# Kernel tuning notes

Hardware: AMD Instinct MI355X
Metric: run time of the kernel (lower is better)

The kernel has to match this reference:

```python
import jax, jax.numpy as jnp
import numpy as np

B, T, N, O = 128, 256, 64, 32
E, H = 32, 64            # embed_dim, hyper_dim
S = O * 4 + 1            # state_dim = 129


def setup_inputs() -> dict:
    key = jax.random.key(0)
    ks = jax.random.split(key, 16)
    def lin(k, i, o):
        return jax.random.normal(k, (i, o), jnp.float32) * (1.0 / np.sqrt(i))
    inp = {}
    inp["agent_qs"] = jax.random.normal(ks[0], (B, T, N), jnp.float32)
    inp["obs"] = jax.random.normal(ks[1], (B, T, N, O), jnp.float32)
    inp["agent_mask"] = jax.random.randint(ks[2], (B, N), 0, 2).astype(jnp.int32)
    # hyper_w_1: Linear(S,H) -> ReLU -> Linear(H, N*E)
    inp["w1_1"] = lin(ks[3], S, H); inp["b1_1"] = jnp.zeros((H,), jnp.float32)
    inp["w1_2"] = lin(ks[4], H, N * E); inp["b1_2"] = jnp.zeros((N * E,), jnp.float32)
    # hyper_w_2: Linear(S,H) -> ReLU -> Linear(H, E)
    inp["w2_1"] = lin(ks[5], S, H); inp["b2_1"] = jnp.zeros((H,), jnp.float32)
    inp["w2_2"] = lin(ks[6], H, E); inp["b2_2"] = jnp.zeros((E,), jnp.float32)
    # hyper_b_1: Linear(S,E)
    inp["wb1"] = lin(ks[7], S, E); inp["bb1"] = jnp.zeros((E,), jnp.float32)
    # hyper_b_2: Linear(S,E) -> ReLU -> Linear(E,1)
    inp["wb2_1"] = lin(ks[8], S, E); inp["bb2_1"] = jnp.zeros((E,), jnp.float32)
    inp["wb2_2"] = lin(ks[9], E, 1); inp["bb2_2"] = jnp.zeros((1,), jnp.float32)
    return inp


def _state_features(obs, agent_mask):
    # Faithful to torch loop: stats over the FIRST k agents where k = mask.sum().
    b, t, n, o = obs.shape
    k = agent_mask.sum(axis=1)                                   # [B]
    am = (jnp.arange(n)[None, :] < k[:, None]).astype(obs.dtype)  # [B,N]
    m = am[:, None, :, None]                                      # [B,1,N,1]
    cnt = k.astype(obs.dtype)[:, None, None]                      # [B,1,1]
    safe = jnp.maximum(cnt, 1.0)
    mean = (obs * m).sum(axis=2) / safe                           # [B,T,O]
    var = (((obs - mean[:, :, None, :]) ** 2) * m).sum(axis=2) / jnp.maximum(cnt - 1.0, 1.0)
    std = jnp.where(cnt > 1.0, jnp.sqrt(var), 0.0)                # unbiased std, 0 if k<=1
    mb = m > 0
    mn = jnp.where(mb, obs, jnp.inf).min(axis=2)
    mx = jnp.where(mb, obs, -jnp.inf).max(axis=2)
    ratio = jnp.broadcast_to(cnt / n, (b, t, 1))
    feats = jnp.concatenate([mean, std, mn, mx, ratio], axis=-1)  # [B,T,S]
    return jnp.where(cnt > 0.0, feats, 0.0)                       # rows stay zero if k==0


def reference(agent_qs, obs, agent_mask,
              w1_1, b1_1, w1_2, b1_2,
              w2_1, b2_1, w2_2, b2_2,
              wb1, bb1, wb2_1, bb2_1, wb2_2, bb2_2):
    b, t, n = agent_qs.shape
    e = wb1.shape[1]
    states = _state_features(obs, agent_mask)                     # [B,T,S]
    s = states.reshape(b * t, -1)                                 # [BT,S]
    qs = agent_qs.reshape(b * t, n)                               # [BT,N]
    w1 = jnp.abs(jax.nn.relu(s @ w1_1 + b1_1) @ w1_2 + b1_2).reshape(b * t, n, e)
    b1 = s @ wb1 + bb1                                            # [BT,E]
    hidden = jax.nn.elu(jnp.einsum('bn,bne->be', qs, w1) + b1)    # [BT,E]
    w2 = jnp.abs(jax.nn.relu(s @ w2_1 + b2_1) @ w2_2 + b2_2)      # [BT,E]
    b2 = jax.nn.relu(s @ wb2_1 + bb2_1) @ wb2_2 + bb2_2           # [BT,1]
    q_tot = (hidden * w2).sum(axis=-1, keepdims=True) + b2        # [BT,1]
    return q_tot.reshape(b, t, 1)
```

## Files before the change

kernel.cpp:

```cpp
#include <hip/hip_runtime.h>
#include <math.h>

#define BB 128
#define TT 256
#define NN 64
#define OO 32
#define EE 32
#define HH 64
#define SS 129
#define BT 32768
#define SP 132

__global__ __launch_bounds__(256) void k_states(const float* __restrict__ obs,
                                                const int* __restrict__ mask,
                                                float* __restrict__ states) {
    int w = threadIdx.x >> 6;
    int l = threadIdx.x & 63;
    int bt = blockIdx.x * 4 + w;
    int b = bt >> 8;

    int kv = mask[(b << 6) + l];
    #pragma unroll
    for (int off = 32; off; off >>= 1) kv += __shfl_xor(kv, off);

    int o = l & 31, nh = l >> 5;
    float sum = 0.f, ssq = 0.f, mn = INFINITY, mx = -INFINITY;
    const float* op = obs + ((size_t)bt << 11);
    for (int n = nh; n < kv; n += 2) {
        float v = op[(n << 5) + o];
        sum += v;
        ssq = fmaf(v, v, ssq);
        mn = fminf(mn, v);
        mx = fmaxf(mx, v);
    }
    sum += __shfl_xor(sum, 32);
    ssq += __shfl_xor(ssq, 32);
    mn = fminf(mn, __shfl_xor(mn, 32));
    mx = fmaxf(mx, __shfl_xor(mx, 32));

    float kf = (float)kv;
    float mean = sum / fmaxf(kf, 1.f);
    float var = (ssq - kf * mean * mean) / fmaxf(kf - 1.f, 1.f);
    float sd = (kv > 1) ? sqrtf(fmaxf(var, 0.f)) : 0.f;
    if (kv == 0) { mean = 0.f; sd = 0.f; mn = 0.f; mx = 0.f; }

    float* sp = states + (size_t)bt * SP;
    if (l < 32) {
        sp[o] = mean;
        sp[32 + o] = sd;
        sp[64 + o] = mn;
        sp[96 + o] = mx;
    }
    if (l == 0) {
        sp[128] = kf * 0.015625f;
        sp[129] = 0.f; sp[130] = 0.f; sp[131] = 0.f;
    }
}

__global__ __launch_bounds__(256) void k_mlp1(const float* __restrict__ states,
        const float* __restrict__ w1_1, const float* __restrict__ b1_1,
        const float* __restrict__ w2_1, const float* __restrict__ b2_1,
        const float* __restrict__ wb1,  const float* __restrict__ bb1,
        const float* __restrict__ wb2_1,const float* __restrict__ bb2_1,
        float* __restrict__ h1, float* __restrict__ t2,
        float* __restrict__ b1v, float* __restrict__ t3) {
    __shared__ float wl[SP * 192];
    __shared__ float bl[192];
    int t = threadIdx.x;

    for (int idx = t; idx < SP * 192; idx += 256) {
        int k = idx / 192;
        int c = idx - k * 192;
        float v = 0.f;
        if (k < SS) {
            if (c < 64)       v = w1_1[k * 64 + c];
            else if (c < 128) v = w2_1[k * 64 + c - 64];
            else if (c < 160) v = wb1[k * 32 + c - 128];
            else              v = wb2_1[k * 32 + c - 160];
        }
        wl[idx] = v;
    }
    if (t < 192) {
        float v;
        if (t < 64)       v = b1_1[t];
        else if (t < 128) v = b2_1[t - 64];
        else if (t < 160) v = bb1[t - 128];
        else              v = bb2_1[t - 160];
        bl[t] = v;
    }
    __syncthreads();

    int cg = t & 7, rg = t >> 3;
    int c0 = cg * 24;
    int row0 = blockIdx.x * 128 + rg * 4;
    float acc[4][24];
    #pragma unroll
    for (int i = 0; i < 4; i++)
        #pragma unroll
        for (int j = 0; j < 24; j++) acc[i][j] = 0.f;

    const float* s0 = states + (size_t)row0 * SP;
    for (int k0 = 0; k0 < SP; k0 += 4) {
        float4 sv[4];
        #pragma unroll
        for (int i = 0; i < 4; i++) sv[i] = *(const float4*)(s0 + i * SP + k0);
        #pragma unroll
        for (int kk = 0; kk < 4; kk++) {
            float wv[24];
            #pragma unroll
            for (int q = 0; q < 6; q++)
                *(float4*)&wv[q * 4] = *(const float4*)&wl[(k0 + kk) * 192 + c0 + q * 4];
            #pragma unroll
            for (int i = 0; i < 4; i++) {
                float s = ((const float*)&sv[i])[kk];
                #pragma unroll
                for (int j = 0; j < 24; j++) acc[i][j] = fmaf(s, wv[j], acc[i][j]);
            }
        }
    }

    #pragma unroll
    for (int i = 0; i < 4; i++) {
        int row = row0 + i;
        #pragma unroll
        for (int j = 0; j < 24; j++) {
            int c = c0 + j;
            float v = acc[i][j] + bl[c];
            if (c < 128 || c >= 160) v = fmaxf(v, 0.f);
            if (c < 64)       h1[(size_t)row * 64 + c] = v;
            else if (c < 128) t2[(size_t)row * 64 + c - 64] = v;
            else if (c < 160) b1v[(size_t)row * 32 + c - 128] = v;
            else              t3[(size_t)row * 32 + c - 160] = v;
        }
    }
}

__global__ __launch_bounds__(256) void k_w2(const float* __restrict__ t2,
        const float* __restrict__ t3, const float* __restrict__ w2_2,
        const float* __restrict__ b2_2, const float* __restrict__ wb2_2,
        const float* __restrict__ bb2_2,
        float* __restrict__ w2, float* __restrict__ b2v) {
    __shared__ float wl[64 * 32];
    __shared__ float wb[32];
    __shared__ float bb[32];
    int t = threadIdx.x;
    for (int idx = t; idx < 2048; idx += 256) wl[idx] = w2_2[idx];
    if (t < 32) wb[t] = wb2_2[t];
    if (t >= 32 && t < 64) bb[t - 32] = b2_2[t - 32];
    __syncthreads();

    int r = t >> 2, eq = t & 3;
    int row = blockIdx.x * 64 + r;
    int e0 = eq * 8;
    float acc[8];
    #pragma unroll
    for (int j = 0; j < 8; j++) acc[j] = 0.f;

    const float* tp = t2 + (size_t)row * 64;
    for (int h4 = 0; h4 < 64; h4 += 4) {
        float4 tv = *(const float4*)(tp + h4);
        #pragma unroll
        for (int hh = 0; hh < 4; hh++) {
            float s = ((const float*)&tv)[hh];
            float4 wv0 = *(const float4*)&wl[(h4 + hh) * 32 + e0];
            float4 wv1 = *(const float4*)&wl[(h4 + hh) * 32 + e0 + 4];
            acc[0] = fmaf(s, wv0.x, acc[0]); acc[1] = fmaf(s, wv0.y, acc[1]);
            acc[2] = fmaf(s, wv0.z, acc[2]); acc[3] = fmaf(s, wv0.w, acc[3]);
            acc[4] = fmaf(s, wv1.x, acc[4]); acc[5] = fmaf(s, wv1.y, acc[5]);
            acc[6] = fmaf(s, wv1.z, acc[6]); acc[7] = fmaf(s, wv1.w, acc[7]);
        }
    }
    #pragma unroll
    for (int j = 0; j < 8; j++)
        w2[(size_t)row * 32 + e0 + j] = fabsf(acc[j] + bb[e0 + j]);

    if (eq == 0) {
        const float* t3p = t3 + (size_t)row * 32;
        float a = 0.f;
        #pragma unroll
        for (int q = 0; q < 8; q++) {
            float4 v3 = *(const float4*)(t3p + q * 4);
            float4 wv = *(const float4*)&wb[q * 4];
            a = fmaf(v3.x, wv.x, a); a = fmaf(v3.y, wv.y, a);
            a = fmaf(v3.z, wv.z, a); a = fmaf(v3.w, wv.w, a);
        }
        b2v[row] = a + bb2_2[0];
    }
}

__global__ __launch_bounds__(256, 1) void k_main(
        const float* __restrict__ h1g, const float* __restrict__ qsg,
        const float* __restrict__ w12, const float* __restrict__ b12,
        const float* __restrict__ b1vg, const float* __restrict__ w2g,
        const float* __restrict__ b2vg, float* __restrict__ out) {
    __shared__ float sm[36864];
    float* h1T = sm;
    float* Wp  = sm + 8192;
    float* qsT = sm + 24576;
    float* hid = sm + 32768;

    int t = threadIdx.x;
    int row0 = blockIdx.x * 128;

    {
        int r = t >> 1, h0 = (t & 1) * 32;
        const float* hp = h1g + (size_t)(row0 + r) * 64 + h0;
        const float* qp = qsg + (size_t)(row0 + r) * 64 + h0;
        #pragma unroll
        for (int q = 0; q < 8; q++) {
            float4 hv = *(const float4*)(hp + q * 4);
            float4 qv = *(const float4*)(qp + q * 4);
            int hb = h0 + q * 4;
            h1T[(hb + 0) * 128 + r] = hv.x; h1T[(hb + 1) * 128 + r] = hv.y;
            h1T[(hb + 2) * 128 + r] = hv.z; h1T[(hb + 3) * 128 + r] = hv.w;
            qsT[(hb + 0) * 128 + r] = qv.x; qsT[(hb + 1) * 128 + r] = qv.y;
            qsT[(hb + 2) * 128 + r] = qv.z; qsT[(hb + 3) * 128 + r] = qv.w;
        }
    }

    int rg = t >> 4, cg = t & 15;
    int n_l = cg >> 1, eh = cg & 1;
    int r0 = rg * 8;
    int e0 = eh * 16;
    int jbase = n_l * 32 + e0;
    int xorc = n_l << 2;

    float hacc[8][16];
    #pragma unroll
    for (int i = 0; i < 8; i++)
        #pragma unroll
        for (int jj = 0; jj < 16; jj++) hacc[i][jj] = 0.f;

    for (int p = 0; p < 8; ++p) {
        __syncthreads();
        {
            int c4 = (t & 63) * 4;
            int hh0 = t >> 6;
            int csw = c4 ^ (((c4 >> 5) & 7) << 2);
            const float* wsrc = w12 + (size_t)hh0 * 2048 + p * 256 + c4;
            #pragma unroll
            for (int hh = 0; hh < 16; ++hh) {
                float4 wv = *(const float4*)(wsrc + (size_t)hh * 4 * 2048);
                *(float4*)&Wp[(hh * 4 + hh0) * 256 + csw] = wv;
            }
        }
        __syncthreads();

        int n = p * 8 + n_l;
        float c[8][16];
        {
            float biasv[16];
            #pragma unroll
            for (int q = 0; q < 4; q++)
                *(float4*)&biasv[q * 4] = *(const float4*)(b12 + n * 32 + e0 + q * 4);
            #pragma unroll
            for (int i = 0; i < 8; i++)
                #pragma unroll
                for (int jj = 0; jj < 16; jj++) c[i][jj] = biasv[jj];
        }

        #pragma unroll 2
        for (int k = 0; k < 64; k++) {
            float a[8], w[16];
            *(float4*)&a[0] = *(const float4*)&h1T[k * 128 + r0];
            *(float4*)&a[4] = *(const float4*)&h1T[k * 128 + r0 + 4];
            #pragma unroll
            for (int q = 0; q < 4; q++) {
                int j = (jbase + q * 4) ^ xorc;
                *(float4*)&w[q * 4] = *(const float4*)&Wp[k * 256 + j];
            }
            #pragma unroll
            for (int i = 0; i < 8; i++)
                #pragma unroll
                for (int jj = 0; jj < 16; jj++)
                    c[i][jj] = fmaf(a[i], w[jj], c[i][jj]);
        }

        float qv[8];
        *(float4*)&qv[0] = *(const float4*)&qsT[n * 128 + r0];
        *(float4*)&qv[4] = *(const float4*)&qsT[n * 128 + r0 + 4];
        #pragma unroll
        for (int i = 0; i < 8; i++)
            #pragma unroll
            for (int jj = 0; jj < 16; jj++)
                hacc[i][jj] = fmaf(qv[i], fabsf(c[i][jj]), hacc[i][jj]);
    }

    #pragma unroll
    for (int i = 0; i < 8; i++)
        #pragma unroll
        for (int jj = 0; jj < 16; jj++) {
            float v = hacc[i][jj];
            v += __shfl_xor(v, 2);
            v += __shfl_xor(v, 4);
            v += __shfl_xor(v, 8);
            hacc[i][jj] = v;
        }

    if (n_l == 0) {
        #pragma unroll
        for (int i = 0; i < 8; i++)
            #pragma unroll
            for (int q = 0; q < 4; q++) {
                float4 v = make_float4(hacc[i][q * 4], hacc[i][q * 4 + 1],
                                       hacc[i][q * 4 + 2], hacc[i][q * 4 + 3]);
                *(float4*)&hid[(r0 + i) * 32 + e0 + q * 4] = v;
            }
    }
    __syncthreads();

    {
        int r = t >> 1, half = t & 1, he0 = half * 16;
        int row = row0 + r;
        const float* b1p = b1vg + (size_t)row * 32 + he0;
        const float* w2p = w2g + (size_t)row * 32 + he0;
        float accp = 0.f;
        #pragma unroll
        for (int q = 0; q < 4; q++) {
            float4 hv = *(const float4*)&hid[r * 32 + he0 + q * 4];
            float4 bv = *(const float4*)(b1p + q * 4);
            float4 wv = *(const float4*)(w2p + q * 4);
            float x;
            x = hv.x + bv.x; x = x > 0.f ? x : expm1f(x); accp = fmaf(x, wv.x, accp);
            x = hv.y + bv.y; x = x > 0.f ? x : expm1f(x); accp = fmaf(x, wv.y, accp);
            x = hv.z + bv.z; x = x > 0.f ? x : expm1f(x); accp = fmaf(x, wv.z, accp);
            x = hv.w + bv.w; x = x > 0.f ? x : expm1f(x); accp = fmaf(x, wv.w, accp);
        }
        accp += __shfl_xor(accp, 1);
        if (half == 0) out[row] = accp + b2vg[row];
    }
}

extern "C" void kernel_launch(void* const* d_in, const int* in_sizes, int n_in,
                              void* d_out, int out_size, void* d_ws, size_t ws_size,
                              hipStream_t stream) {
    const float* agent_qs = (const float*)d_in[0];
    const float* obs      = (const float*)d_in[1];
    const int*   agent_mask = (const int*)d_in[2];
    const float* w1_1 = (const float*)d_in[3];
    const float* b1_1 = (const float*)d_in[4];
    const float* w1_2 = (const float*)d_in[5];
    const float* b1_2 = (const float*)d_in[6];
    const float* w2_1 = (const float*)d_in[7];
    const float* b2_1 = (const float*)d_in[8];
    const float* w2_2 = (const float*)d_in[9];
    const float* b2_2 = (const float*)d_in[10];
    const float* wb1  = (const float*)d_in[11];
    const float* bb1  = (const float*)d_in[12];
    const float* wb2_1 = (const float*)d_in[13];
    const float* bb2_1 = (const float*)d_in[14];
    const float* wb2_2 = (const float*)d_in[15];
    const float* bb2_2 = (const float*)d_in[16];

    float* ws = (float*)d_ws;
    float* states = ws;
    float* h1  = states + (size_t)BT * SP;
    float* t2  = h1  + (size_t)BT * 64;
    float* b1v = t2  + (size_t)BT * 64;
    float* t3  = b1v + (size_t)BT * 32;
    float* w2  = t3  + (size_t)BT * 32;
    float* b2v = w2  + (size_t)BT * 32;
    float* outp = (float*)d_out;

    k_states<<<BT / 4, 256, 0, stream>>>(obs, agent_mask, states);
    k_mlp1<<<BT / 128, 256, 0, stream>>>(states, w1_1, b1_1, w2_1, b2_1,
                                         wb1, bb1, wb2_1, bb2_1, h1, t2, b1v, t3);
    k_w2<<<BT / 64, 256, 0, stream>>>(t2, t3, w2_2, b2_2, wb2_2, bb2_2, w2, b2v);
    k_main<<<BT / 128, 256, 0, stream>>>(h1, agent_qs, w1_2, b1_2, b1v, w2, b2v, outp);
}
```

Baseline: 611.5 us.

## Shrink per-block tiles in mlp1 and main kernels to raise occupancy

Splits k_mlp1 across a second grid dimension so each block computes 96 output columns instead of 192, which halves LDS and register use and allows 3 blocks per CU. Restructures k_main to process 64 rows per block with 4x4 register tiles and 2 agents per pass (32 passes), dropping the qs transpose and LDS swizzle and reading qs directly from global memory. The aim is higher occupancy for better latency hiding. In exchange the weight tiles are reloaded more often, states are read twice, and each thread reuses fewer operands.

```diff
diff --git a/kernel.cpp b/kernel.cpp
--- a/kernel.cpp
+++ b/kernel.cpp
@@ -57,64 +57,62 @@
     }
 }
 
-__global__ __launch_bounds__(256) void k_mlp1(const float* __restrict__ states,
+__global__ __launch_bounds__(256, 3) void k_mlp1(const float* __restrict__ states,
         const float* __restrict__ w1_1, const float* __restrict__ b1_1,
         const float* __restrict__ w2_1, const float* __restrict__ b2_1,
         const float* __restrict__ wb1,  const float* __restrict__ bb1,
         const float* __restrict__ wb2_1,const float* __restrict__ bb2_1,
         float* __restrict__ h1, float* __restrict__ t2,
         float* __restrict__ b1v, float* __restrict__ t3) {
-    __shared__ float wl[SP * 192];
-    __shared__ float bl[192];
+    __shared__ float wl[SP * 96];
+    __shared__ float bl[96];
     int t = threadIdx.x;
-
-    for (int idx = t; idx < SP * 192; idx += 256) {
-        int k = idx / 192;
-        int c = idx - k * 192;
+    int half = blockIdx.y;
+
+    const float* wA = half ? w2_1 : w1_1;
+    const float* wB = half ? wb2_1 : wb1;
+    const float* bA = half ? b2_1 : b1_1;
+    const float* bB = half ? bb2_1 : bb1;
+    float* outA = half ? t2 : h1;
+    float* outB = half ? t3 : b1v;
+    int reluB = half;
+
+    for (int idx = t; idx < SP * 96; idx += 256) {
+        int k = idx / 96;
+        int c = idx - k * 96;
         float v = 0.f;
-        if (k < SS) {
-            if (c < 64)       v = w1_1[k * 64 + c];
-            else if (c < 128) v = w2_1[k * 64 + c - 64];
-            else if (c < 160) v = wb1[k * 32 + c - 128];
-            else              v = wb2_1[k * 32 + c - 160];
-        }
+        if (k < SS) v = (c < 64) ? wA[k * 64 + c] : wB[k * 32 + (c - 64)];
         wl[idx] = v;
     }
-    if (t < 192) {
-        float v;
-        if (t < 64)       v = b1_1[t];
-        else if (t < 128) v = b2_1[t - 64];
-        else if (t < 160) v = bb1[t - 128];
-        else              v = bb2_1[t - 160];
-        bl[t] = v;
-    }
+    if (t < 96) bl[t] = (t < 64) ? bA[t] : bB[t - 64];
     __syncthreads();
 
     int cg = t & 7, rg = t >> 3;
-    int c0 = cg * 24;
+    int c0 = cg * 12;
     int row0 = blockIdx.x * 128 + rg * 4;
-    float acc[4][24];
+    float acc[4][12];
     #pragma unroll
     for (int i = 0; i < 4; i++)
         #pragma unroll
-        for (int j = 0; j < 24; j++) acc[i][j] = 0.f;
+        for (int j = 0; j < 12; j++) acc[i][j] = 0.f;
 
     const float* s0 = states + (size_t)row0 * SP;
     for (int k0 = 0; k0 < SP; k0 += 4) {
-        float4 sv[4];
-        #pragma unroll
-        for (int i = 0; i < 4; i++) sv[i] = *(const float4*)(s0 + i * SP + k0);
+        float sv[4][4];
+        #pragma unroll
+        for (int i = 0; i < 4; i++)
+            *(float4*)&sv[i][0] = *(const float4*)(s0 + i * SP + k0);
         #pragma unroll
         for (int kk = 0; kk < 4; kk++) {
-            float wv[24];
-            #pragma unroll
-            for (int q = 0; q < 6; q++)
-                *(float4*)&wv[q * 4] = *(const float4*)&wl[(k0 + kk) * 192 + c0 + q * 4];
+            float wv[12];
+            #pragma unroll
+            for (int q = 0; q < 3; q++)
+                *(float4*)&wv[q * 4] = *(const float4*)&wl[(k0 + kk) * 96 + c0 + q * 4];
             #pragma unroll
             for (int i = 0; i < 4; i++) {
-                float s = ((const float*)&sv[i])[kk];
+                float s = sv[i][kk];
                 #pragma unroll
-                for (int j = 0; j < 24; j++) acc[i][j] = fmaf(s, wv[j], acc[i][j]);
+                for (int j = 0; j < 12; j++) acc[i][j] = fmaf(s, wv[j], acc[i][j]);
             }
         }
     }
@@ -123,14 +121,16 @@
     for (int i = 0; i < 4; i++) {
         int row = row0 + i;
         #pragma unroll
-        for (int j = 0; j < 24; j++) {
+        for (int j = 0; j < 12; j++) {
             int c = c0 + j;
             float v = acc[i][j] + bl[c];
-            if (c < 128 || c >= 160) v = fmaxf(v, 0.f);
-            if (c < 64)       h1[(size_t)row * 64 + c] = v;
-            else if (c < 128) t2[(size_t)row * 64 + c - 64] = v;
-            else if (c < 160) b1v[(size_t)row * 32 + c - 128] = v;
-            else              t3[(size_t)row * 32 + c - 160] = v;
+            if (c < 64) {
+                v = fmaxf(v, 0.f);
+                outA[(size_t)row * 64 + c] = v;
+            } else {
+                if (reluB) v = fmaxf(v, 0.f);
+                outB[(size_t)row * 32 + (c - 64)] = v;
+            }
         }
     }
 }
@@ -158,10 +158,11 @@
 
     const float* tp = t2 + (size_t)row * 64;
     for (int h4 = 0; h4 < 64; h4 += 4) {
-        float4 tv = *(const float4*)(tp + h4);
+        float tv[4];
+        *(float4*)tv = *(const float4*)(tp + h4);
         #pragma unroll
         for (int hh = 0; hh < 4; hh++) {
-            float s = ((const float*)&tv)[hh];
+            float s = tv[hh];
             float4 wv0 = *(const float4*)&wl[(h4 + hh) * 32 + e0];
             float4 wv1 = *(const float4*)&wl[(h4 + hh) * 32 + e0 + 4];
             acc[0] = fmaf(s, wv0.x, acc[0]); acc[1] = fmaf(s, wv0.y, acc[1]);
@@ -188,135 +189,116 @@
     }
 }
 
-__global__ __launch_bounds__(256, 1) void k_main(
+__global__ __launch_bounds__(256, 4) void k_main(
         const float* __restrict__ h1g, const float* __restrict__ qsg,
         const float* __restrict__ w12, const float* __restrict__ b12,
         const float* __restrict__ b1vg, const float* __restrict__ w2g,
         const float* __restrict__ b2vg, float* __restrict__ out) {
-    __shared__ float sm[36864];
-    float* h1T = sm;
-    float* Wp  = sm + 8192;
-    float* qsT = sm + 24576;
-    float* hid = sm + 32768;
-
+    __shared__ float h1T[64 * 64];
+    __shared__ float Wp[64 * 64];
+    __shared__ float hid[64 * 32];
     int t = threadIdx.x;
-    int row0 = blockIdx.x * 128;
+    int row0 = blockIdx.x * 64;
 
     {
-        int r = t >> 1, h0 = (t & 1) * 32;
+        int r = t >> 2, h0 = (t & 3) * 16;
         const float* hp = h1g + (size_t)(row0 + r) * 64 + h0;
-        const float* qp = qsg + (size_t)(row0 + r) * 64 + h0;
-        #pragma unroll
-        for (int q = 0; q < 8; q++) {
+        #pragma unroll
+        for (int q = 0; q < 4; q++) {
             float4 hv = *(const float4*)(hp + q * 4);
-            float4 qv = *(const float4*)(qp + q * 4);
             int hb = h0 + q * 4;
-            h1T[(hb + 0) * 128 + r] = hv.x; h1T[(hb + 1) * 128 + r] = hv.y;
-            h1T[(hb + 2) * 128 + r] = hv.z; h1T[(hb + 3) * 128 + r] = hv.w;
-            qsT[(hb + 0) * 128 + r] = qv.x; qsT[(hb + 1) * 128 + r] = qv.y;
-            qsT[(hb + 2) * 128 + r] = qv.z; qsT[(hb + 3) * 128 + r] = qv.w;
+            h1T[(hb + 0) * 64 + r] = hv.x;
+            h1T[(hb + 1) * 64 + r] = hv.y;
+            h1T[(hb + 2) * 64 + r] = hv.z;
+            h1T[(hb + 3) * 64 + r] = hv.w;
         }
     }
 
     int rg = t >> 4, cg = t & 15;
-    int n_l = cg >> 1, eh = cg & 1;
-    int r0 = rg * 8;
-    int e0 = eh * 16;
-    int jbase = n_l * 32 + e0;
-    int xorc = n_l << 2;
-
-    float hacc[8][16];
-    #pragma unroll
-    for (int i = 0; i < 8; i++)
-        #pragma unroll
-        for (int jj = 0; jj < 16; jj++) hacc[i][jj] = 0.f;
-
-    for (int p = 0; p < 8; ++p) {
+    int n_l = cg >> 3;
+    int e0 = (cg & 7) * 4;
+    int r0 = rg * 4;
+    int jcol = n_l * 32 + e0;
+
+    float hacc[4][4];
+    #pragma unroll
+    for (int i = 0; i < 4; i++)
+        #pragma unroll
+        for (int j = 0; j < 4; j++) hacc[i][j] = 0.f;
+
+    for (int p = 0; p < 32; ++p) {
         __syncthreads();
         {
-            int c4 = (t & 63) * 4;
-            int hh0 = t >> 6;
-            int csw = c4 ^ (((c4 >> 5) & 7) << 2);
-            const float* wsrc = w12 + (size_t)hh0 * 2048 + p * 256 + c4;
-            #pragma unroll
-            for (int hh = 0; hh < 16; ++hh) {
-                float4 wv = *(const float4*)(wsrc + (size_t)hh * 4 * 2048);
-                *(float4*)&Wp[(hh * 4 + hh0) * 256 + csw] = wv;
-            }
+            int h = t >> 4, c4 = (t & 15) * 4;
+            const float* wsrc = w12 + (size_t)h * 2048 + p * 64 + c4;
+            float4 wv[4];
+            #pragma unroll
+            for (int q = 0; q < 4; q++)
+                wv[q] = *(const float4*)(wsrc + (size_t)q * 16 * 2048);
+            #pragma unroll
+            for (int q = 0; q < 4; q++)
+                *(float4*)&Wp[(h + q * 16) * 64 + c4] = wv[q];
         }
         __syncthreads();
 
-        int n = p * 8 + n_l;
-        float c[8][16];
+        int n = p * 2 + n_l;
+        float qv[4];
+        #pragma unroll
+        for (int i = 0; i < 4; i++)
+            qv[i] = qsg[(size_t)(row0 + r0 + i) * 64 + n];
+
+        float c[4][4];
         {
-            float biasv[16];
-            #pragma unroll
-            for (int q = 0; q < 4; q++)
-                *(float4*)&biasv[q * 4] = *(const float4*)(b12 + n * 32 + e0 + q * 4);
-            #pragma unroll
-            for (int i = 0; i < 8; i++)
+            float bvv[4];
+            *(float4*)bvv = *(const float4*)(b12 + n * 32 + e0);
+            #pragma unroll
+            for (int i = 0; i < 4; i++)
                 #pragma unroll
-                for (int jj = 0; jj < 16; jj++) c[i][jj] = biasv[jj];
-        }
-
-        #pragma unroll 2
+                for (int j = 0; j < 4; j++) c[i][j] = bvv[j];
+        }
+
+        #pragma unroll
         for (int k = 0; k < 64; k++) {
-            float a[8], w[16];
-            *(float4*)&a[0] = *(const float4*)&h1T[k * 128 + r0];
-            *(float4*)&a[4] = *(const float4*)&h1T[k * 128 + r0 + 4];
-            #pragma unroll
-            for (int q = 0; q < 4; q++) {
-                int j = (jbase + q * 4) ^ xorc;
-                *(float4*)&w[q * 4] = *(const float4*)&Wp[k * 256 + j];
-            }
-            #pragma unroll
-            for (int i = 0; i < 8; i++)
+            float a[4], w[4];
+            *(float4*)a = *(const float4*)&h1T[k * 64 + r0];
+            *(float4*)w = *(const float4*)&Wp[k * 64 + jcol];
+            #pragma unroll
+            for (int i = 0; i < 4; i++)
                 #pragma unroll
-                for (int jj = 0; jj < 16; jj++)
-                    c[i][jj] = fmaf(a[i], w[jj], c[i][jj]);
-        }
-
-        float qv[8];
-        *(float4*)&qv[0] = *(const float4*)&qsT[n * 128 + r0];
-        *(float4*)&qv[4] = *(const float4*)&qsT[n * 128 + r0 + 4];
-        #pragma unroll
-        for (int i = 0; i < 8; i++)
-            #pragma unroll
-            for (int jj = 0; jj < 16; jj++)
-                hacc[i][jj] = fmaf(qv[i], fabsf(c[i][jj]), hacc[i][jj]);
-    }
-
-    #pragma unroll
-    for (int i = 0; i < 8; i++)
-        #pragma unroll
-        for (int jj = 0; jj < 16; jj++) {
-            float v = hacc[i][jj];
-            v += __shfl_xor(v, 2);
-            v += __shfl_xor(v, 4);
-            v += __shfl_xor(v, 8);
-            hacc[i][jj] = v;
-        }
+                for (int j = 0; j < 4; j++)
+                    c[i][j] = fmaf(a[i], w[j], c[i][j]);
+        }
+
+        #pragma unroll
+        for (int i = 0; i < 4; i++)
+            #pragma unroll
+            for (int j = 0; j < 4; j++)
+                hacc[i][j] = fmaf(qv[i], fabsf(c[i][j]), hacc[i][j]);
+    }
+
+    #pragma unroll
+    for (int i = 0; i < 4; i++)
+        #pragma unroll
+        for (int j = 0; j < 4; j++)
+            hacc[i][j] += __shfl_xor(hacc[i][j], 8);
 
     if (n_l == 0) {
         #pragma unroll
-        for (int i = 0; i < 8; i++)
-            #pragma unroll
-            for (int q = 0; q < 4; q++) {
-                float4 v = make_float4(hacc[i][q * 4], hacc[i][q * 4 + 1],
-                                       hacc[i][q * 4 + 2], hacc[i][q * 4 + 3]);
-                *(float4*)&hid[(r0 + i) * 32 + e0 + q * 4] = v;
-            }
+        for (int i = 0; i < 4; i++) {
+            float4 v = make_float4(hacc[i][0], hacc[i][1], hacc[i][2], hacc[i][3]);
+            *(float4*)&hid[(r0 + i) * 32 + e0] = v;
+        }
     }
     __syncthreads();
 
     {
-        int r = t >> 1, half = t & 1, he0 = half * 16;
+        int r = t >> 2, eq = t & 3, he0 = eq * 8;
         int row = row0 + r;
         const float* b1p = b1vg + (size_t)row * 32 + he0;
         const float* w2p = w2g + (size_t)row * 32 + he0;
         float accp = 0.f;
         #pragma unroll
-        for (int q = 0; q < 4; q++) {
+        for (int q = 0; q < 2; q++) {
             float4 hv = *(const float4*)&hid[r * 32 + he0 + q * 4];
             float4 bv = *(const float4*)(b1p + q * 4);
             float4 wv = *(const float4*)(w2p + q * 4);
@@ -327,7 +309,8 @@
             x = hv.w + bv.w; x = x > 0.f ? x : expm1f(x); accp = fmaf(x, wv.w, accp);
         }
         accp += __shfl_xor(accp, 1);
-        if (half == 0) out[row] = accp + b2vg[row];
+        accp += __shfl_xor(accp, 2);
+        if (eq == 0) out[row] = accp + b2vg[row];
     }
 }
 
@@ -363,8 +346,9 @@
     float* outp = (float*)d_out;
 
     k_states<<<BT / 4, 256, 0, stream>>>(obs, agent_mask, states);
-    k_mlp1<<<BT / 128, 256, 0, stream>>>(states, w1_1, b1_1, w2_1, b2_1,
-                                         wb1, bb1, wb2_1, bb2_1, h1, t2, b1v, t3);
+    dim3 g1(BT / 128, 2);
+    k_mlp1<<<g1, 256, 0, stream>>>(states, w1_1, b1_1, w2_1, b2_1,
+                                   wb1, bb1, wb2_1, bb2_1, h1, t2, b1v, t3);
     k_w2<<<BT / 64, 256, 0, stream>>>(t2, t3, w2_2, b2_2, wb2_2, bb2_2, w2, b2v);
-    k_main<<<BT / 128, 256, 0, stream>>>(h1, agent_qs, w1_2, b1_2, b1v, w2, b2v, outp);
-}
+    k_main<<<BT / 64, 256, 0, stream>>>(h1, agent_qs, w1_2, b1_2, b1v, w2, b2v, outp);
+}
```

After: 559.9 us. 8.4% less time.
